# Optimization experiments

Measured on AMD Instinct MI355X. Metric: run time of the kernel, lower is better.

The kernel has to match this reference:

```python
import jax, jax.numpy as jnp
import numpy as np

N_NODES = 50000
N_EDGES = 640000
HIDDEN = 128
NUM_CONVS = 3
VOCAB = 100  # nn.Embedding(100, hidden_dim)


def setup_inputs() -> dict:
    key = jax.random.key(0)
    ks = jax.random.split(key, 8)
    z = jax.random.randint(ks[0], (N_NODES,), 0, VOCAB)
    edge_index = jax.random.randint(ks[1], (2, N_EDGES), 0, N_NODES)
    edge_attr = jax.random.normal(ks[2], (N_EDGES, HIDDEN), jnp.float32)
    emb = jax.random.normal(ks[3], (VOCAB, HIDDEN), jnp.float32) * 0.02
    s = 1.0 / np.sqrt(HIDDEN)
    # Stacked per-conv MLP params: Linear(H,H) -> relu -> Linear(H,H)
    W1 = jax.random.uniform(ks[4], (NUM_CONVS, HIDDEN, HIDDEN), jnp.float32, -s, s)
    b1 = jnp.zeros((NUM_CONVS, HIDDEN), jnp.float32)
    W2 = jax.random.uniform(ks[5], (NUM_CONVS, HIDDEN, HIDDEN), jnp.float32, -s, s)
    b2 = jnp.zeros((NUM_CONVS, HIDDEN), jnp.float32)
    return dict(z=z, edge_index=edge_index, edge_attr=edge_attr,
                emb=emb, W1=W1, b1=b1, W2=W2, b2=b2)


def reference(z, edge_index, edge_attr, emb, W1, b1, W2, b2):
    x = emb[z]  # [N, H] node embeddings
    src, dst = edge_index[0], edge_index[1]
    n = x.shape[0]
    num_convs = W1.shape[0]
    for i in range(num_convs):
        # GINEConv: message = relu(x_j + edge_attr), aggr='add' at dst
        msg = jax.nn.relu(x[src] + edge_attr)                      # [E, H]
        agg = jax.ops.segment_sum(msg, dst, num_segments=n)        # [N, H]
        out = agg + x  # (1 + eps) * x_r with eps = 0
        # MultiLayerPerceptron(H, [H, H], activation='relu'): relu between layers only
        h = jax.nn.relu(out @ W1[i] + b1[i]) @ W2[i] + b2[i]
        if i < num_convs - 1:
            h = jax.nn.relu(h)  # inter-conv activation
        x = h + x  # short_cut residual
    return x  # concat_hidden=False -> last hidden
```

## Files before the change

kernel.cpp:

```cpp
#include <hip/hip_runtime.h>

#define HID 128
#define NNODE 50000
#define NEDGE 640000

typedef __attribute__((ext_vector_type(8))) short bf16x8;
typedef __attribute__((ext_vector_type(4))) float f32x4;

static __global__ void embed_kernel(const int* __restrict__ z,
                                    const float* __restrict__ emb,
                                    float* __restrict__ x) {
  int i = blockIdx.x * 256 + threadIdx.x;
  const int total = NNODE * (HID / 4);
  if (i >= total) return;
  int node = i >> 5;
  int c = i & 31;
  ((float4*)x)[i] = ((const float4*)emb)[(size_t)z[node] * 32 + c];
}

static __global__ void hist_kernel(const int* __restrict__ dst, int* __restrict__ deg) {
  int i = blockIdx.x * 256 + threadIdx.x;
  if (i < NEDGE) atomicAdd(&deg[dst[i]], 1);
}

static __global__ void scan_kernel(const int* __restrict__ deg,
                                   int* __restrict__ row_ptr,
                                   int* __restrict__ cursor) {
  __shared__ int sums[1024];
  int t = threadIdx.x;
  const int per = (NNODE + 1023) / 1024;
  int base = t * per;
  int s = 0;
  for (int i = 0; i < per; ++i) {
    int idx = base + i;
    if (idx < NNODE) s += deg[idx];
  }
  sums[t] = s;
  __syncthreads();
  for (int off = 1; off < 1024; off <<= 1) {
    int v = (t >= off) ? sums[t - off] : 0;
    __syncthreads();
    if (t >= off) sums[t] += v;
    __syncthreads();
  }
  int run = (t == 0) ? 0 : sums[t - 1];
  for (int i = 0; i < per; ++i) {
    int idx = base + i;
    if (idx < NNODE) {
      row_ptr[idx] = run;
      cursor[idx] = run;
      run += deg[idx];
    }
  }
  if (t == 1023) row_ptr[NNODE] = run;
}

static __global__ void fill_kernel(const int* __restrict__ src, const int* __restrict__ dst,
                                   int* __restrict__ cursor, int2* __restrict__ elist) {
  int i = blockIdx.x * 256 + threadIdx.x;
  if (i < NEDGE) {
    int d = dst[i];
    int p = atomicAdd(&cursor[d], 1);
    elist[p] = make_int2(i, src[i]);
  }
}

static __global__ void wsplit_kernel(const float* __restrict__ W1, const float* __restrict__ W2,
                                     unsigned short* __restrict__ whi,
                                     unsigned short* __restrict__ wlo) {
  int idx = blockIdx.x * 256 + threadIdx.x;
  if (idx >= 6 * 16384) return;
  int cg = idx >> 14;
  int rem = idx & 16383;
  int k = rem >> 7, n = rem & 127;
  int c = cg >> 1, g = cg & 1;
  float v = (g ? W2 : W1)[c * 16384 + k * 128 + n];
  unsigned u = __float_as_uint(v);
  unsigned hb = u >> 16;
  float hf = __uint_as_float(hb << 16);
  unsigned lb = __float_as_uint(v - hf) >> 16;
  int o = cg * 17408 + n * 136 + k;
  whi[o] = (unsigned short)hb;
  wlo[o] = (unsigned short)lb;
}

static __global__ __launch_bounds__(256) void gather_kernel(
    const float* __restrict__ x, const float* __restrict__ ea,
    const int* __restrict__ row_ptr, const int2* __restrict__ elist,
    float* __restrict__ out) {
  const int tid = threadIdx.x;
  const int wave = tid >> 6;
  const int lane = tid & 63;
  const int half = lane >> 5;
  const int li = lane & 31;
  const int node = blockIdx.x * 8 + wave * 2 + half;
  const f32x4* x4 = (const f32x4*)x;
  const f32x4* e4 = (const f32x4*)ea;

  f32x4 a0 = (f32x4){0.f, 0.f, 0.f, 0.f};
  f32x4 a1 = (f32x4){0.f, 0.f, 0.f, 0.f};
  f32x4 a2 = (f32x4){0.f, 0.f, 0.f, 0.f};
  f32x4 a3 = (f32x4){0.f, 0.f, 0.f, 0.f};
  int j = 0, je = 0;
  if (node < NNODE) {
    j = row_ptr[node];
    je = row_ptr[node + 1];
    a0 = x4[(size_t)node * 32 + li];
  }
  for (; j + 4 <= je; j += 4) {
    int2 e0 = elist[j];
    int2 e1 = elist[j + 1];
    int2 e2 = elist[j + 2];
    int2 e3 = elist[j + 3];
    f32x4 xv0 = x4[(size_t)e0.y * 32 + li];
    f32x4 ev0 = __builtin_nontemporal_load(&e4[(size_t)e0.x * 32 + li]);
    f32x4 xv1 = x4[(size_t)e1.y * 32 + li];
    f32x4 ev1 = __builtin_nontemporal_load(&e4[(size_t)e1.x * 32 + li]);
    f32x4 xv2 = x4[(size_t)e2.y * 32 + li];
    f32x4 ev2 = __builtin_nontemporal_load(&e4[(size_t)e2.x * 32 + li]);
    f32x4 xv3 = x4[(size_t)e3.y * 32 + li];
    f32x4 ev3 = __builtin_nontemporal_load(&e4[(size_t)e3.x * 32 + li]);
#pragma unroll
    for (int q = 0; q < 4; ++q) {
      a0[q] += fmaxf(xv0[q] + ev0[q], 0.f);
      a1[q] += fmaxf(xv1[q] + ev1[q], 0.f);
      a2[q] += fmaxf(xv2[q] + ev2[q], 0.f);
      a3[q] += fmaxf(xv3[q] + ev3[q], 0.f);
    }
  }
  if (j + 2 <= je) {
    int2 e0 = elist[j];
    int2 e1 = elist[j + 1];
    f32x4 xv0 = x4[(size_t)e0.y * 32 + li];
    f32x4 ev0 = __builtin_nontemporal_load(&e4[(size_t)e0.x * 32 + li]);
    f32x4 xv1 = x4[(size_t)e1.y * 32 + li];
    f32x4 ev1 = __builtin_nontemporal_load(&e4[(size_t)e1.x * 32 + li]);
#pragma unroll
    for (int q = 0; q < 4; ++q) {
      a0[q] += fmaxf(xv0[q] + ev0[q], 0.f);
      a1[q] += fmaxf(xv1[q] + ev1[q], 0.f);
    }
    j += 2;
  }
  if (j < je) {
    int2 e0 = elist[j];
    f32x4 xv0 = x4[(size_t)e0.y * 32 + li];
    f32x4 ev0 = __builtin_nontemporal_load(&e4[(size_t)e0.x * 32 + li]);
#pragma unroll
    for (int q = 0; q < 4; ++q) a0[q] += fmaxf(xv0[q] + ev0[q], 0.f);
  }
  if (node < NNODE) {
#pragma unroll
    for (int q = 0; q < 4; ++q) a0[q] += a1[q] + a2[q] + a3[q];
    ((f32x4*)out)[(size_t)node * 32 + li] = a0;
  }
}

static __global__ __launch_bounds__(256) void mlp_mfma(
    const float* __restrict__ in, const float* __restrict__ xres,
    const unsigned short* __restrict__ wt1hi, const unsigned short* __restrict__ wt1lo,
    const unsigned short* __restrict__ wt2hi, const unsigned short* __restrict__ wt2lo,
    const float* __restrict__ b1, const float* __restrict__ b2,
    float* __restrict__ xout, int relu_out) {
  __shared__ unsigned short WbHi[128 * 72];
  __shared__ unsigned short WbLo[128 * 72];
  __shared__ float Ts[64 * 132];
  const int tid = threadIdx.x;
  const int w = tid >> 6, l = tid & 63;
  const int lm = l & 15, quad = l >> 4;
  const int row0 = blockIdx.x * 64;

  float b1v[8], b2v[8];
#pragma unroll
  for (int t = 0; t < 8; ++t) { b1v[t] = b1[t * 16 + lm]; b2v[t] = b2[t * 16 + lm]; }

  f32x4 acc[8];
#pragma unroll
  for (int t = 0; t < 8; ++t) acc[t] = (f32x4){0.f, 0.f, 0.f, 0.f};

  int arow = row0 + w * 16 + lm;
  if (arow >= NNODE) arow = NNODE - 1;

  for (int kc = 0; kc < 128; kc += 64) {
    __syncthreads();
    for (int idx = tid; idx < 128 * 8; idx += 256) {
      int n = idx >> 3, seg = idx & 7;
      *(uint4*)&WbHi[n * 72 + seg * 8] = *(const uint4*)&wt1hi[n * 136 + kc + seg * 8];
      *(uint4*)&WbLo[n * 72 + seg * 8] = *(const uint4*)&wt1lo[n * 136 + kc + seg * 8];
    }
    __syncthreads();
#pragma unroll
    for (int ks = 0; ks < 64; ks += 32) {
      const float* ap = in + (size_t)arow * 128 + kc + ks + quad * 8;
      float4 av0 = *(const float4*)ap;
      float4 av1 = *(const float4*)(ap + 4);
      float av[8] = {av0.x, av0.y, av0.z, av0.w, av1.x, av1.y, av1.z, av1.w};
      bf16x8 ah, al;
#pragma unroll
      for (int jj = 0; jj < 8; ++jj) {
        unsigned u = __float_as_uint(av[jj]);
        unsigned hb = u >> 16;
        float hf = __uint_as_float(hb << 16);
        unsigned lb = __float_as_uint(av[jj] - hf) >> 16;
        ah[jj] = (short)hb; al[jj] = (short)lb;
      }
#pragma unroll
      for (int t = 0; t < 8; ++t) {
        int off = (t * 16 + lm) * 72 + ks + quad * 8;
        bf16x8 bh = *(const bf16x8*)&WbHi[off];
        bf16x8 bl = *(const bf16x8*)&WbLo[off];
        acc[t] = __builtin_amdgcn_mfma_f32_16x16x32_bf16(ah, bh, acc[t], 0, 0, 0);
        acc[t] = __builtin_amdgcn_mfma_f32_16x16x32_bf16(ah, bl, acc[t], 0, 0, 0);
        acc[t] = __builtin_amdgcn_mfma_f32_16x16x32_bf16(al, bh, acc[t], 0, 0, 0);
      }
    }
  }
  __syncthreads();

#pragma unroll
  for (int t = 0; t < 8; ++t)
#pragma unroll
    for (int r = 0; r < 4; ++r)
      Ts[(w * 16 + quad * 4 + r) * 132 + t * 16 + lm] = fmaxf(acc[t][r] + b1v[t], 0.f);

#pragma unroll
  for (int t = 0; t < 8; ++t) acc[t] = (f32x4){0.f, 0.f, 0.f, 0.f};
  __syncthreads();

  for (int kc = 0; kc < 128; kc += 64) {
    __syncthreads();
    for (int idx = tid; idx < 128 * 8; idx += 256) {
      int n = idx >> 3, seg = idx & 7;
      *(uint4*)&WbHi[n * 72 + seg * 8] = *(const uint4*)&wt2hi[n * 136 + kc + seg * 8];
      *(uint4*)&WbLo[n * 72 + seg * 8] = *(const uint4*)&wt2lo[n * 136 + kc + seg * 8];
    }
    __syncthreads();
#pragma unroll
    for (int ks = 0; ks < 64; ks += 32) {
      const float* tp = &Ts[(w * 16 + lm) * 132 + kc + ks + quad * 8];
      float4 av0 = *(const float4*)tp;
      float4 av1 = *(const float4*)(tp + 4);
      float av[8] = {av0.x, av0.y, av0.z, av0.w, av1.x, av1.y, av1.z, av1.w};
      bf16x8 ah, al;
#pragma unroll
      for (int jj = 0; jj < 8; ++jj) {
        unsigned u = __float_as_uint(av[jj]);
        unsigned hb = u >> 16;
        float hf = __uint_as_float(hb << 16);
        unsigned lb = __float_as_uint(av[jj] - hf) >> 16;
        ah[jj] = (short)hb; al[jj] = (short)lb;
      }
#pragma unroll
      for (int t = 0; t < 8; ++t) {
        int off = (t * 16 + lm) * 72 + ks + quad * 8;
        bf16x8 bh = *(const bf16x8*)&WbHi[off];
        bf16x8 bl = *(const bf16x8*)&WbLo[off];
        acc[t] = __builtin_amdgcn_mfma_f32_16x16x32_bf16(ah, bh, acc[t], 0, 0, 0);
        acc[t] = __builtin_amdgcn_mfma_f32_16x16x32_bf16(ah, bl, acc[t], 0, 0, 0);
        acc[t] = __builtin_amdgcn_mfma_f32_16x16x32_bf16(al, bh, acc[t], 0, 0, 0);
      }
    }
  }

#pragma unroll
  for (int t = 0; t < 8; ++t) {
#pragma unroll
    for (int r = 0; r < 4; ++r) {
      int row = row0 + w * 16 + quad * 4 + r;
      if (row < NNODE) {
        int col = t * 16 + lm;
        float v = acc[t][r] + b2v[t];
        if (relu_out) v = fmaxf(v, 0.f);
        v += xres[(size_t)row * 128 + col];
        xout[(size_t)row * 128 + col] = v;
      }
    }
  }
}

extern "C" void kernel_launch(void* const* d_in, const int* in_sizes, int n_in,
                              void* d_out, int out_size, void* d_ws, size_t ws_size,
                              hipStream_t stream) {
  const int*   z   = (const int*)d_in[0];
  const int*   ei  = (const int*)d_in[1];
  const float* ea  = (const float*)d_in[2];
  const float* emb = (const float*)d_in[3];
  const float* W1  = (const float*)d_in[4];
  const float* b1  = (const float*)d_in[5];
  const float* W2  = (const float*)d_in[6];
  const float* b2  = (const float*)d_in[7];
  float* outp = (float*)d_out;

  char* ws = (char*)d_ws;
  float* xbuf   = (float*)(ws + 0);
  float* obuf   = (float*)(ws + 25600000);
  int*   deg    = (int*)  (ws + 51200000);
  int*   cursor = (int*)  (ws + 51400000);
  int*   rowptr = (int*)  (ws + 51600000);
  int2*  elist  = (int2*) (ws + 51800016);
  unsigned short* whi = (unsigned short*)(ws + 57000000);
  unsigned short* wlo = (unsigned short*)(ws + 57250000);

  const int* srcv = ei;
  const int* dstv = ei + NEDGE;

  hipMemsetAsync(deg, 0, NNODE * sizeof(int), stream);
  embed_kernel<<<(NNODE * 32 + 255) / 256, 256, 0, stream>>>(z, emb, xbuf);
  hist_kernel<<<(NEDGE + 255) / 256, 256, 0, stream>>>(dstv, deg);
  scan_kernel<<<1, 1024, 0, stream>>>(deg, rowptr, cursor);
  fill_kernel<<<(NEDGE + 255) / 256, 256, 0, stream>>>(srcv, dstv, cursor, elist);
  wsplit_kernel<<<(6 * 16384 + 255) / 256, 256, 0, stream>>>(W1, W2, whi, wlo);

  for (int i = 0; i < 3; ++i) {
    gather_kernel<<<(NNODE + 7) / 8, 256, 0, stream>>>(xbuf, ea, rowptr, elist, obuf);
    float* xo = (i == 2) ? outp : xbuf;
    mlp_mfma<<<(NNODE + 63) / 64, 256, 0, stream>>>(
        obuf, xbuf,
        whi + (size_t)(i * 2 + 0) * 17408, wlo + (size_t)(i * 2 + 0) * 17408,
        whi + (size_t)(i * 2 + 1) * 17408, wlo + (size_t)(i * 2 + 1) * 17408,
        b1 + (size_t)i * HID, b2 + (size_t)i * HID,
        xo, (i < 2) ? 1 : 0);
  }
}
```

Before: 975.9 us.

## Fuse edge gather into MLP kernel and vectorize the degree scan

Merges the per-node edge aggregation into the MFMA MLP kernel. Each 64-row block gathers its nodes' messages straight into shared memory, which removes the intermediate aggregate write and read through global memory and one launch per conv. Because the input and output x now differ, the code ping-pongs x between two buffers. The scan kernel now reads and writes degrees with int4 vector accesses. Risks: the gather now runs at the MLP's block granularity with less parallelism per block, and the larger fused kernel may lose occupancy.

```diff
diff --git a/kernel.cpp b/kernel.cpp
--- a/kernel.cpp
+++ b/kernel.cpp
@@ -28,12 +28,20 @@
                                    int* __restrict__ cursor) {
   __shared__ int sums[1024];
   int t = threadIdx.x;
-  const int per = (NNODE + 1023) / 1024;
+  const int per = 52;
   int base = t * per;
   int s = 0;
-  for (int i = 0; i < per; ++i) {
-    int idx = base + i;
-    if (idx < NNODE) s += deg[idx];
+  if (base + per <= NNODE) {
+#pragma unroll
+    for (int i = 0; i < per; i += 4) {
+      int4 v = *(const int4*)&deg[base + i];
+      s += v.x + v.y + v.z + v.w;
+    }
+  } else {
+    for (int i = 0; i < per; ++i) {
+      int idx = base + i;
+      if (idx < NNODE) s += deg[idx];
+    }
   }
   sums[t] = s;
   __syncthreads();
@@ -44,15 +52,25 @@
     __syncthreads();
   }
   int run = (t == 0) ? 0 : sums[t - 1];
-  for (int i = 0; i < per; ++i) {
-    int idx = base + i;
-    if (idx < NNODE) {
-      row_ptr[idx] = run;
-      cursor[idx] = run;
-      run += deg[idx];
-    }
-  }
-  if (t == 1023) row_ptr[NNODE] = run;
+  if (base + per <= NNODE) {
+#pragma unroll
+    for (int i = 0; i < per; i += 4) {
+      int4 v = *(const int4*)&deg[base + i];
+      int4 rp;
+      rp.x = run; run += v.x;
+      rp.y = run; run += v.y;
+      rp.z = run; run += v.z;
+      rp.w = run; run += v.w;
+      *(int4*)&row_ptr[base + i] = rp;
+      *(int4*)&cursor[base + i] = rp;
+    }
+  } else {
+    for (int i = 0; i < per; ++i) {
+      int idx = base + i;
+      if (idx < NNODE) { row_ptr[idx] = run; cursor[idx] = run; run += deg[idx]; }
+    }
+  }
+  if (t == 1023) row_ptr[NNODE] = sums[1023];
 }
 
 static __global__ void fill_kernel(const int* __restrict__ src, const int* __restrict__ dst,
@@ -84,80 +102,9 @@
   wlo[o] = (unsigned short)lb;
 }
 
-static __global__ __launch_bounds__(256) void gather_kernel(
+static __global__ __launch_bounds__(256) void conv_fused(
     const float* __restrict__ x, const float* __restrict__ ea,
     const int* __restrict__ row_ptr, const int2* __restrict__ elist,
-    float* __restrict__ out) {
-  const int tid = threadIdx.x;
-  const int wave = tid >> 6;
-  const int lane = tid & 63;
-  const int half = lane >> 5;
-  const int li = lane & 31;
-  const int node = blockIdx.x * 8 + wave * 2 + half;
-  const f32x4* x4 = (const f32x4*)x;
-  const f32x4* e4 = (const f32x4*)ea;
-
-  f32x4 a0 = (f32x4){0.f, 0.f, 0.f, 0.f};
-  f32x4 a1 = (f32x4){0.f, 0.f, 0.f, 0.f};
-  f32x4 a2 = (f32x4){0.f, 0.f, 0.f, 0.f};
-  f32x4 a3 = (f32x4){0.f, 0.f, 0.f, 0.f};
-  int j = 0, je = 0;
-  if (node < NNODE) {
-    j = row_ptr[node];
-    je = row_ptr[node + 1];
-    a0 = x4[(size_t)node * 32 + li];
-  }
-  for (; j + 4 <= je; j += 4) {
-    int2 e0 = elist[j];
-    int2 e1 = elist[j + 1];
-    int2 e2 = elist[j + 2];
-    int2 e3 = elist[j + 3];
-    f32x4 xv0 = x4[(size_t)e0.y * 32 + li];
-    f32x4 ev0 = __builtin_nontemporal_load(&e4[(size_t)e0.x * 32 + li]);
-    f32x4 xv1 = x4[(size_t)e1.y * 32 + li];
-    f32x4 ev1 = __builtin_nontemporal_load(&e4[(size_t)e1.x * 32 + li]);
-    f32x4 xv2 = x4[(size_t)e2.y * 32 + li];
-    f32x4 ev2 = __builtin_nontemporal_load(&e4[(size_t)e2.x * 32 + li]);
-    f32x4 xv3 = x4[(size_t)e3.y * 32 + li];
-    f32x4 ev3 = __builtin_nontemporal_load(&e4[(size_t)e3.x * 32 + li]);
-#pragma unroll
-    for (int q = 0; q < 4; ++q) {
-      a0[q] += fmaxf(xv0[q] + ev0[q], 0.f);
-      a1[q] += fmaxf(xv1[q] + ev1[q], 0.f);
-      a2[q] += fmaxf(xv2[q] + ev2[q], 0.f);
-      a3[q] += fmaxf(xv3[q] + ev3[q], 0.f);
-    }
-  }
-  if (j + 2 <= je) {
-    int2 e0 = elist[j];
-    int2 e1 = elist[j + 1];
-    f32x4 xv0 = x4[(size_t)e0.y * 32 + li];
-    f32x4 ev0 = __builtin_nontemporal_load(&e4[(size_t)e0.x * 32 + li]);
-    f32x4 xv1 = x4[(size_t)e1.y * 32 + li];
-    f32x4 ev1 = __builtin_nontemporal_load(&e4[(size_t)e1.x * 32 + li]);
-#pragma unroll
-    for (int q = 0; q < 4; ++q) {
-      a0[q] += fmaxf(xv0[q] + ev0[q], 0.f);
-      a1[q] += fmaxf(xv1[q] + ev1[q], 0.f);
-    }
-    j += 2;
-  }
-  if (j < je) {
-    int2 e0 = elist[j];
-    f32x4 xv0 = x4[(size_t)e0.y * 32 + li];
-    f32x4 ev0 = __builtin_nontemporal_load(&e4[(size_t)e0.x * 32 + li]);
-#pragma unroll
-    for (int q = 0; q < 4; ++q) a0[q] += fmaxf(xv0[q] + ev0[q], 0.f);
-  }
-  if (node < NNODE) {
-#pragma unroll
-    for (int q = 0; q < 4; ++q) a0[q] += a1[q] + a2[q] + a3[q];
-    ((f32x4*)out)[(size_t)node * 32 + li] = a0;
-  }
-}
-
-static __global__ __launch_bounds__(256) void mlp_mfma(
-    const float* __restrict__ in, const float* __restrict__ xres,
     const unsigned short* __restrict__ wt1hi, const unsigned short* __restrict__ wt1lo,
     const unsigned short* __restrict__ wt2hi, const unsigned short* __restrict__ wt2lo,
     const float* __restrict__ b1, const float* __restrict__ b2,
@@ -168,8 +115,80 @@
   const int tid = threadIdx.x;
   const int w = tid >> 6, l = tid & 63;
   const int lm = l & 15, quad = l >> 4;
+  const int hw = tid >> 5;
+  const int li = tid & 31;
   const int row0 = blockIdx.x * 64;
 
+#define STAGE(HP, LP, KC)                                                        \
+  for (int idx = tid; idx < 128 * 8; idx += 256) {                               \
+    int n_ = idx >> 3, seg_ = idx & 7;                                           \
+    *(uint4*)&WbHi[n_ * 72 + seg_ * 8] = *(const uint4*)&HP[n_ * 136 + (KC) + seg_ * 8]; \
+    *(uint4*)&WbLo[n_ * 72 + seg_ * 8] = *(const uint4*)&LP[n_ * 136 + (KC) + seg_ * 8]; \
+  }
+
+  STAGE(wt1hi, wt1lo, 0)
+
+  {
+    const f32x4* x4 = (const f32x4*)x;
+    const f32x4* e4 = (const f32x4*)ea;
+    for (int nl = hw; nl < 64; nl += 8) {
+      int node = row0 + nl;
+      f32x4 a0 = (f32x4){0.f, 0.f, 0.f, 0.f};
+      f32x4 a1 = a0, a2 = a0, a3 = a0;
+      int j = 0, je = 0;
+      if (node < NNODE) {
+        j = row_ptr[node];
+        je = row_ptr[node + 1];
+        a0 = x4[(size_t)node * 32 + li];
+      }
+      for (; j + 4 <= je; j += 4) {
+        int2 e0 = elist[j];
+        int2 e1 = elist[j + 1];
+        int2 e2 = elist[j + 2];
+        int2 e3 = elist[j + 3];
+        f32x4 xv0 = x4[(size_t)e0.y * 32 + li];
+        f32x4 ev0 = __builtin_nontemporal_load(&e4[(size_t)e0.x * 32 + li]);
+        f32x4 xv1 = x4[(size_t)e1.y * 32 + li];
+        f32x4 ev1 = __builtin_nontemporal_load(&e4[(size_t)e1.x * 32 + li]);
+        f32x4 xv2 = x4[(size_t)e2.y * 32 + li];
+        f32x4 ev2 = __builtin_nontemporal_load(&e4[(size_t)e2.x * 32 + li]);
+        f32x4 xv3 = x4[(size_t)e3.y * 32 + li];
+        f32x4 ev3 = __builtin_nontemporal_load(&e4[(size_t)e3.x * 32 + li]);
+#pragma unroll
+        for (int q = 0; q < 4; ++q) {
+          a0[q] += fmaxf(xv0[q] + ev0[q], 0.f);
+          a1[q] += fmaxf(xv1[q] + ev1[q], 0.f);
+          a2[q] += fmaxf(xv2[q] + ev2[q], 0.f);
+          a3[q] += fmaxf(xv3[q] + ev3[q], 0.f);
+        }
+      }
+      if (j + 2 <= je) {
+        int2 e0 = elist[j];
+        int2 e1 = elist[j + 1];
+        f32x4 xv0 = x4[(size_t)e0.y * 32 + li];
+        f32x4 ev0 = __builtin_nontemporal_load(&e4[(size_t)e0.x * 32 + li]);
+        f32x4 xv1 = x4[(size_t)e1.y * 32 + li];
+        f32x4 ev1 = __builtin_nontemporal_load(&e4[(size_t)e1.x * 32 + li]);
+#pragma unroll
+        for (int q = 0; q < 4; ++q) {
+          a0[q] += fmaxf(xv0[q] + ev0[q], 0.f);
+          a1[q] += fmaxf(xv1[q] + ev1[q], 0.f);
+        }
+        j += 2;
+      }
+      if (j < je) {
+        int2 e0 = elist[j];
+        f32x4 xv0 = x4[(size_t)e0.y * 32 + li];
+        f32x4 ev0 = __builtin_nontemporal_load(&e4[(size_t)e0.x * 32 + li]);
+#pragma unroll
+        for (int q = 0; q < 4; ++q) a0[q] += fmaxf(xv0[q] + ev0[q], 0.f);
+      }
+#pragma unroll
+      for (int q = 0; q < 4; ++q) a0[q] += a1[q] + a2[q] + a3[q];
+      *(f32x4*)&Ts[nl * 132 + li * 4] = a0;
+    }
+  }
+
   float b1v[8], b2v[8];
 #pragma unroll
   for (int t = 0; t < 8; ++t) { b1v[t] = b1[t * 16 + lm]; b2v[t] = b2[t * 16 + lm]; }
@@ -178,43 +197,40 @@
 #pragma unroll
   for (int t = 0; t < 8; ++t) acc[t] = (f32x4){0.f, 0.f, 0.f, 0.f};
 
-  int arow = row0 + w * 16 + lm;
-  if (arow >= NNODE) arow = NNODE - 1;
-
-  for (int kc = 0; kc < 128; kc += 64) {
-    __syncthreads();
-    for (int idx = tid; idx < 128 * 8; idx += 256) {
-      int n = idx >> 3, seg = idx & 7;
-      *(uint4*)&WbHi[n * 72 + seg * 8] = *(const uint4*)&wt1hi[n * 136 + kc + seg * 8];
-      *(uint4*)&WbLo[n * 72 + seg * 8] = *(const uint4*)&wt1lo[n * 136 + kc + seg * 8];
-    }
-    __syncthreads();
-#pragma unroll
-    for (int ks = 0; ks < 64; ks += 32) {
-      const float* ap = in + (size_t)arow * 128 + kc + ks + quad * 8;
-      float4 av0 = *(const float4*)ap;
-      float4 av1 = *(const float4*)(ap + 4);
-      float av[8] = {av0.x, av0.y, av0.z, av0.w, av1.x, av1.y, av1.z, av1.w};
-      bf16x8 ah, al;
-#pragma unroll
-      for (int jj = 0; jj < 8; ++jj) {
-        unsigned u = __float_as_uint(av[jj]);
-        unsigned hb = u >> 16;
-        float hf = __uint_as_float(hb << 16);
-        unsigned lb = __float_as_uint(av[jj] - hf) >> 16;
-        ah[jj] = (short)hb; al[jj] = (short)lb;
-      }
-#pragma unroll
-      for (int t = 0; t < 8; ++t) {
-        int off = (t * 16 + lm) * 72 + ks + quad * 8;
-        bf16x8 bh = *(const bf16x8*)&WbHi[off];
-        bf16x8 bl = *(const bf16x8*)&WbLo[off];
-        acc[t] = __builtin_amdgcn_mfma_f32_16x16x32_bf16(ah, bh, acc[t], 0, 0, 0);
-        acc[t] = __builtin_amdgcn_mfma_f32_16x16x32_bf16(ah, bl, acc[t], 0, 0, 0);
-        acc[t] = __builtin_amdgcn_mfma_f32_16x16x32_bf16(al, bh, acc[t], 0, 0, 0);
-      }
-    }
-  }
+  __syncthreads();
+
+#define GEMM_CHUNK(KC)                                                           \
+  _Pragma("unroll")                                                              \
+  for (int ks = 0; ks < 64; ks += 32) {                                          \
+    const float* tp = &Ts[(w * 16 + lm) * 132 + (KC) + ks + quad * 8];           \
+    float4 av0 = *(const float4*)tp;                                             \
+    float4 av1 = *(const float4*)(tp + 4);                                       \
+    float av[8] = {av0.x, av0.y, av0.z, av0.w, av1.x, av1.y, av1.z, av1.w};      \
+    bf16x8 ah, al;                                                               \
+    _Pragma("unroll")                                                            \
+    for (int jj = 0; jj < 8; ++jj) {                                             \
+      unsigned u = __float_as_uint(av[jj]);                                      \
+      unsigned hb = u >> 16;                                                     \
+      float hf = __uint_as_float(hb << 16);                                      \
+      unsigned lb = __float_as_uint(av[jj] - hf) >> 16;                          \
+      ah[jj] = (short)hb; al[jj] = (short)lb;                                    \
+    }                                                                            \
+    _Pragma("unroll")                                                            \
+    for (int t = 0; t < 8; ++t) {                                                \
+      int off = (t * 16 + lm) * 72 + ks + quad * 8;                              \
+      bf16x8 bh = *(const bf16x8*)&WbHi[off];                                    \
+      bf16x8 bl = *(const bf16x8*)&WbLo[off];                                    \
+      acc[t] = __builtin_amdgcn_mfma_f32_16x16x32_bf16(ah, bh, acc[t], 0, 0, 0); \
+      acc[t] = __builtin_amdgcn_mfma_f32_16x16x32_bf16(ah, bl, acc[t], 0, 0, 0); \
+      acc[t] = __builtin_amdgcn_mfma_f32_16x16x32_bf16(al, bh, acc[t], 0, 0, 0); \
+    }                                                                            \
+  }
+
+  GEMM_CHUNK(0)
+  __syncthreads();
+  STAGE(wt1hi, wt1lo, 64)
+  __syncthreads();
+  GEMM_CHUNK(64)
   __syncthreads();
 
 #pragma unroll
@@ -227,40 +243,13 @@
   for (int t = 0; t < 8; ++t) acc[t] = (f32x4){0.f, 0.f, 0.f, 0.f};
   __syncthreads();
 
-  for (int kc = 0; kc < 128; kc += 64) {
-    __syncthreads();
-    for (int idx = tid; idx < 128 * 8; idx += 256) {
-      int n = idx >> 3, seg = idx & 7;
-      *(uint4*)&WbHi[n * 72 + seg * 8] = *(const uint4*)&wt2hi[n * 136 + kc + seg * 8];
-      *(uint4*)&WbLo[n * 72 + seg * 8] = *(const uint4*)&wt2lo[n * 136 + kc + seg * 8];
-    }
-    __syncthreads();
-#pragma unroll
-    for (int ks = 0; ks < 64; ks += 32) {
-      const float* tp = &Ts[(w * 16 + lm) * 132 + kc + ks + quad * 8];
-      float4 av0 = *(const float4*)tp;
-      float4 av1 = *(const float4*)(tp + 4);
-      float av[8] = {av0.x, av0.y, av0.z, av0.w, av1.x, av1.y, av1.z, av1.w};
-      bf16x8 ah, al;
-#pragma unroll
-      for (int jj = 0; jj < 8; ++jj) {
-        unsigned u = __float_as_uint(av[jj]);
-        unsigned hb = u >> 16;
-        float hf = __uint_as_float(hb << 16);
-        unsigned lb = __float_as_uint(av[jj] - hf) >> 16;
-        ah[jj] = (short)hb; al[jj] = (short)lb;
-      }
-#pragma unroll
-      for (int t = 0; t < 8; ++t) {
-        int off = (t * 16 + lm) * 72 + ks + quad * 8;
-        bf16x8 bh = *(const bf16x8*)&WbHi[off];
-        bf16x8 bl = *(const bf16x8*)&WbLo[off];
-        acc[t] = __builtin_amdgcn_mfma_f32_16x16x32_bf16(ah, bh, acc[t], 0, 0, 0);
-        acc[t] = __builtin_amdgcn_mfma_f32_16x16x32_bf16(ah, bl, acc[t], 0, 0, 0);
-        acc[t] = __builtin_amdgcn_mfma_f32_16x16x32_bf16(al, bh, acc[t], 0, 0, 0);
-      }
-    }
-  }
+  STAGE(wt2hi, wt2lo, 0)
+  __syncthreads();
+  GEMM_CHUNK(0)
+  __syncthreads();
+  STAGE(wt2hi, wt2lo, 64)
+  __syncthreads();
+  GEMM_CHUNK(64)
 
 #pragma unroll
   for (int t = 0; t < 8; ++t) {
@@ -271,11 +260,13 @@
         int col = t * 16 + lm;
         float v = acc[t][r] + b2v[t];
         if (relu_out) v = fmaxf(v, 0.f);
-        v += xres[(size_t)row * 128 + col];
+        v += x[(size_t)row * 128 + col];
         xout[(size_t)row * 128 + col] = v;
       }
     }
   }
+#undef STAGE
+#undef GEMM_CHUNK
 }
 
 extern "C" void kernel_launch(void* const* d_in, const int* in_sizes, int n_in,
@@ -311,14 +302,15 @@
   fill_kernel<<<(NEDGE + 255) / 256, 256, 0, stream>>>(srcv, dstv, cursor, elist);
   wsplit_kernel<<<(6 * 16384 + 255) / 256, 256, 0, stream>>>(W1, W2, whi, wlo);
 
+  const float* xin = xbuf;
   for (int i = 0; i < 3; ++i) {
-    gather_kernel<<<(NNODE + 7) / 8, 256, 0, stream>>>(xbuf, ea, rowptr, elist, obuf);
-    float* xo = (i == 2) ? outp : xbuf;
-    mlp_mfma<<<(NNODE + 63) / 64, 256, 0, stream>>>(
-        obuf, xbuf,
+    float* xo = (i == 2) ? outp : ((i == 0) ? obuf : xbuf);
+    conv_fused<<<(NNODE + 63) / 64, 256, 0, stream>>>(
+        xin, ea, rowptr, elist,
         whi + (size_t)(i * 2 + 0) * 17408, wlo + (size_t)(i * 2 + 0) * 17408,
         whi + (size_t)(i * 2 + 1) * 17408, wlo + (size_t)(i * 2 + 1) * 17408,
         b1 + (size_t)i * HID, b2 + (size_t)i * HID,
         xo, (i < 2) ? 1 : 0);
-  }
-}
+    xin = xo;
+  }
+}
```

Result: faster. 938.2 us (-3.9%).
